# Performance work log

Hardware: AMD Instinct MI355X
Metric: run time of the kernel (lower is better)

The kernel has to match this reference:

```python
import jax, jax.numpy as jnp
import numpy as np

N = 100000
FEAT = 256
HID = 128
OUT = 64
E = 1600000


def setup_inputs() -> dict:
    key = jax.random.key(0)
    ks = jax.random.split(key, 8)
    x = jax.random.normal(ks[0], (N, FEAT), dtype=jnp.float32)
    edge_index = jax.random.randint(ks[1], (2, E), 0, N, dtype=jnp.int64)
    # Glorot-like weights, zero bias (PyG GCNConv default init style)
    def glorot(k, fin, fout):
        s = (6.0 / (fin + fout)) ** 0.5
        return jax.random.uniform(k, (fin, fout), jnp.float32, -s, s)
    return {
        "x": x,
        "edge_index": edge_index,
        "W1": glorot(ks[2], FEAT, HID), "b1": jnp.zeros((HID,), jnp.float32),
        "W2": glorot(ks[3], HID, HID), "b2": jnp.zeros((HID,), jnp.float32),
        "W3": glorot(ks[4], HID, OUT), "b3": jnp.zeros((OUT,), jnp.float32),
    }


def _gcn_prep(edge_index, n_nodes):
    # Add self-loops and compute symmetric normalization deg^-1/2 (PyG gcn_norm).
    loops = jnp.arange(n_nodes, dtype=edge_index.dtype)
    src = jnp.concatenate([edge_index[0], loops])
    dst = jnp.concatenate([edge_index[1], loops])
    ones = jnp.ones(src.shape[0], dtype=jnp.float32)
    deg = jax.ops.segment_sum(ones, dst, num_segments=n_nodes)
    dinv = jnp.where(deg > 0, jax.lax.rsqrt(jnp.maximum(deg, 1.0)), 0.0)
    norm = dinv[src] * dinv[dst]  # [E+N]
    return src, dst, norm


def _gcn_layer(x, src, dst, norm, W, b, n_nodes):
    h = x @ W                              # [N, F_out]
    msg = h[src] * norm[:, None]           # gather + edge scale
    out = jax.ops.segment_sum(msg, dst, num_segments=n_nodes)  # scatter-add
    return out + b


def reference(x, edge_index, W1, b1, W2, b2, W3, b3):
    n = x.shape[0]
    src, dst, norm = _gcn_prep(edge_index, n)
    h = jax.nn.relu(_gcn_layer(x, src, dst, norm, W1, b1, n))
    h = jax.nn.relu(_gcn_layer(h, src, dst, norm, W2, b2, n))
    return _gcn_layer(h, src, dst, norm, W3, b3, n)
```

## Files before the change

kernel.cpp:

```cpp
#include <hip/hip_runtime.h>
#include <hip/hip_bf16.h>


#define NNODES 100000
#define NB 391
#define PB 2048
#define BCAP 12288

typedef _Float16 half8  __attribute__((ext_vector_type(8)));
typedef _Float16 half4v __attribute__((ext_vector_type(4)));
typedef _Float16 half2v __attribute__((ext_vector_type(2)));
typedef float    floatx4 __attribute__((ext_vector_type(4)));

static __device__ __forceinline__ floatx4 h2f4(half4v v) {
    return (floatx4){(float)v.x, (float)v.y, (float)v.z, (float)v.w};
}

__global__ __launch_bounds__(256) void blockhist_k(const int* __restrict__ dst,
                                                   int* __restrict__ H, int e) {
    __shared__ int h[NB];
    for (int q = threadIdx.x; q < NB; q += 256) h[q] = 0;
    __syncthreads();
    int base = blockIdx.x * PB;
    int lim = e - base; if (lim > PB) lim = PB;
    for (int i = threadIdx.x; i < lim; i += 256)
        atomicAdd(&h[dst[base + i] >> 8], 1);
    __syncthreads();
    for (int q = threadIdx.x; q < NB; q += 256)
        H[(size_t)blockIdx.x * NB + q] = h[q];
}

__global__ __launch_bounds__(256) void bucketscan_k(const int* __restrict__ H,
                                                    int* __restrict__ O,
                                                    int* __restrict__ T, int npb) {
    __shared__ int lds[256];
    int b = blockIdx.x, t = threadIdx.x;
    int running = 0;
    for (int c0 = 0; c0 < npb; c0 += 256) {
        int idx = c0 + t;
        int v = (idx < npb) ? H[(size_t)idx * NB + b] : 0;
        lds[t] = v;
        __syncthreads();
        #pragma unroll
        for (int off = 1; off < 256; off <<= 1) {
            int u = (t >= off) ? lds[t - off] : 0;
            __syncthreads();
            lds[t] += u;
            __syncthreads();
        }
        int excl = lds[t] - v + running;
        if (idx < npb) O[(size_t)idx * NB + b] = excl;
        running += lds[255];
        __syncthreads();
    }
    if (t == 0) T[b] = running;
}

__global__ __launch_bounds__(512) void scanT_k(const int* __restrict__ T,
                                               int* __restrict__ bbase, int e) {
    __shared__ int lds[512];
    int t = threadIdx.x;
    int v = (t < NB) ? T[t] : 0;
    lds[t] = v;
    __syncthreads();
    #pragma unroll
    for (int off = 1; off < 512; off <<= 1) {
        int u = (t >= off) ? lds[t - off] : 0;
        __syncthreads();
        lds[t] += u;
        __syncthreads();
    }
    if (t < NB) bbase[t] = lds[t] - v;
    if (t == 0) bbase[NB] = e;
}

__global__ __launch_bounds__(256) void scatter_k(const int* __restrict__ src,
                                                 const int* __restrict__ dst,
                                                 const int* __restrict__ O,
                                                 const int* __restrict__ bbase,
                                                 unsigned* __restrict__ binned, int e) {
    __shared__ int cur[NB];
    for (int q = threadIdx.x; q < NB; q += 256)
        cur[q] = bbase[q] + O[(size_t)blockIdx.x * NB + q];
    __syncthreads();
    int base = blockIdx.x * PB;
    int lim = e - base; if (lim > PB) lim = PB;
    for (int i = threadIdx.x; i < lim; i += 256) {
        int d = dst[base + i];
        int s = src[base + i];
        int p = atomicAdd(&cur[d >> 8], 1);
        binned[p] = ((unsigned)(d & 255) << 17) | (unsigned)s;
    }
}

__global__ __launch_bounds__(256) void bucket_fill_k(
    const unsigned* __restrict__ binned, const int* __restrict__ bbase,
    int* __restrict__ rowptr, int* __restrict__ eidx,
    float* __restrict__ dinv, int n, int e) {
    __shared__ int cnt[256];
    __shared__ int cur[256];
    __shared__ int lds[256];
    __shared__ int sbuf[BCAP];
    int b = blockIdx.x, t = threadIdx.x;
    int beg = bbase[b], end = bbase[b + 1];
    int m = end - beg;
    cnt[t] = 0;
    __syncthreads();
    for (int q = t; q < m; q += 256) {
        unsigned r = binned[beg + q];
        atomicAdd(&cnt[r >> 17], 1);
    }
    __syncthreads();
    int v = cnt[t];
    lds[t] = v;
    __syncthreads();
    #pragma unroll
    for (int off = 1; off < 256; off <<= 1) {
        int u = (t >= off) ? lds[t - off] : 0;
        __syncthreads();
        lds[t] += u;
        __syncthreads();
    }
    int excl = lds[t] - v;
    int node = b * 256 + t;
    if (node < n) {
        rowptr[node] = beg + excl;
        dinv[node] = rsqrtf(1.0f + (float)v);
    }
    if (b == NB - 1 && t == 0) rowptr[n] = e;
    cur[t] = excl;
    __syncthreads();
    for (int q = t; q < m; q += 256) {
        unsigned r = binned[beg + q];
        int p = atomicAdd(&cur[r >> 17], 1);
        if (p < BCAP) sbuf[p] = (int)(r & 0x1FFFFu);
    }
    __syncthreads();
    for (int q = t; q < m; q += 256) eidx[beg + q] = sbuf[q];
}

__global__ __launch_bounds__(256) void castWt_k(
    const float* __restrict__ W1, const float* __restrict__ W2,
    const float* __restrict__ W3, _Float16* __restrict__ Wt1,
    _Float16* __restrict__ Wt2, _Float16* __restrict__ Wt3) {
    int i = blockIdx.x * 256 + threadIdx.x;
    if (i < 128 * 256) {
        int nn = i >> 8, k = i & 255;
        Wt1[i] = (_Float16)W1[k * 128 + nn];
    }
    if (i < 128 * 128) {
        int nn = i >> 7, k = i & 127;
        Wt2[i] = (_Float16)W2[k * 128 + nn];
    }
    if (i < 64 * 128) {
        int nn = i >> 7, k = i & 127;
        Wt3[i] = (_Float16)W3[k * 64 + nn];
    }
}

template<typename TA, int FIN, int FOUT>
__global__ __launch_bounds__(256) void gemm_mfma_k(
    const TA* __restrict__ X, const _Float16* __restrict__ Wt,
    const float* __restrict__ dinv, _Float16* __restrict__ G, int n)
{
    constexpr int KC = 64;
    constexpr int KP = 72;
    constexpr int NT = FOUT / 16;
    __shared__ _Float16 xS[128 * KP];

    const int tid  = threadIdx.x;
    const int wave = tid >> 6;
    const int lane = tid & 63;
    const int mrow = lane & 15;
    const int kq   = (lane >> 4) * 8;

    const int m0 = blockIdx.x * 128;
    const int row_s = tid >> 1;
    const int col_s = (tid & 1) * 32;
    int gr = m0 + row_s; if (gr > n - 1) gr = n - 1;

    floatx4 acc[2][NT];
    #pragma unroll
    for (int i = 0; i < 2; ++i)
        #pragma unroll
        for (int j = 0; j < NT; ++j) acc[i][j] = (floatx4){0.f, 0.f, 0.f, 0.f};

    const int lr0 = wave * 32 + mrow;
    const int lr1 = lr0 + 16;

    for (int kc = 0; kc < FIN; kc += KC) {
        if (kc) __syncthreads();
        _Float16* sp = &xS[row_s * KP + col_s];
        if constexpr (sizeof(TA) == 4) {
            const float* xp = (const float*)X + (size_t)gr * FIN + kc + col_s;
            #pragma unroll
            for (int q = 0; q < 4; ++q) {
                float4 u0 = *(const float4*)(xp + q * 8);
                float4 u1 = *(const float4*)(xp + q * 8 + 4);
                *(half8*)(sp + q * 8) =
                    (half8){(_Float16)u0.x, (_Float16)u0.y, (_Float16)u0.z, (_Float16)u0.w,
                            (_Float16)u1.x, (_Float16)u1.y, (_Float16)u1.z, (_Float16)u1.w};
            }
        } else {
            const _Float16* xp = (const _Float16*)X + (size_t)gr * FIN + kc + col_s;
            #pragma unroll
            for (int q = 0; q < 4; ++q)
                *(half8*)(sp + q * 8) = *(const half8*)(xp + q * 8);
        }
        __syncthreads();

        #pragma unroll
        for (int kk = 0; kk < KC; kk += 32) {
            half8 a0 = *(const half8*)&xS[lr0 * KP + kk + kq];
            half8 a1 = *(const half8*)&xS[lr1 * KP + kk + kq];
            #pragma unroll
            for (int ct = 0; ct < NT; ++ct) {
                half8 b = *(const half8*)(Wt + (size_t)(ct * 16 + mrow) * FIN + kc + kk + kq);
                acc[0][ct] = __builtin_amdgcn_mfma_f32_16x16x32_f16(a0, b, acc[0][ct], 0, 0, 0);
                acc[1][ct] = __builtin_amdgcn_mfma_f32_16x16x32_f16(a1, b, acc[1][ct], 0, 0, 0);
            }
        }
    }

    #pragma unroll
    for (int rt = 0; rt < 2; ++rt) {
        #pragma unroll
        for (int reg = 0; reg < 4; ++reg) {
            int r = m0 + wave * 32 + rt * 16 + (lane >> 4) * 4 + reg;
            if (r < n) {
                float s = dinv[r];
                #pragma unroll
                for (int ct = 0; ct < NT; ++ct) {
                    G[(size_t)r * FOUT + ct * 16 + mrow] = (_Float16)(acc[rt][ct][reg] * s);
                }
            }
        }
    }
}

template<bool RELU, typename OutT>
__global__ __launch_bounds__(256) void gather128_k(
    const _Float16* __restrict__ g, const int* __restrict__ rowptr,
    const int* __restrict__ eidx, const float* __restrict__ dinv,
    const float* __restrict__ bias, OutT* __restrict__ out, int n)
{
    int wave = threadIdx.x >> 6;
    int lane = threadIdx.x & 63;
    int half = lane >> 5;
    int hl   = lane & 31;
    int node = blockIdx.x * 4 + wave;
    if (node >= n) return;

    int beg = rowptr[node];
    int end = rowptr[node + 1];

    const half4v* g4 = (const half4v*)g;
    floatx4 aA = {0.f,0.f,0.f,0.f}, aB = aA, aC = aA, aD = aA;
    if (half == 0) aA = h2f4(g4[(size_t)node * 32 + hl]);

    for (int j0 = beg; j0 < end; j0 += 64) {
        int m = end - j0; if (m > 64) m = 64;
        int id = (lane < m) ? eidx[j0 + lane] : 0;
        int t = 0;
        for (; t + 7 < m; t += 8) {
            int i0 = __shfl(id, t + half);
            int i1 = __shfl(id, t + 2 + half);
            int i2 = __shfl(id, t + 4 + half);
            int i3 = __shfl(id, t + 6 + half);
            half4v v0 = g4[(size_t)i0 * 32 + hl];
            half4v v1 = g4[(size_t)i1 * 32 + hl];
            half4v v2 = g4[(size_t)i2 * 32 + hl];
            half4v v3 = g4[(size_t)i3 * 32 + hl];
            aA += h2f4(v0); aB += h2f4(v1); aC += h2f4(v2); aD += h2f4(v3);
        }
        for (; t + 1 < m; t += 2) {
            int i0 = __shfl(id, t + half);
            aA += h2f4(g4[(size_t)i0 * 32 + hl]);
        }
        if (t < m) {
            int i0 = __shfl(id, t);
            if (half == 0) aA += h2f4(g4[(size_t)i0 * 32 + hl]);
        }
    }
    aA += aB; aC += aD; aA += aC;
    aA.x += __shfl_down(aA.x, 32);
    aA.y += __shfl_down(aA.y, 32);
    aA.z += __shfl_down(aA.z, 32);
    aA.w += __shfl_down(aA.w, 32);

    if (half == 0) {
        float sc = dinv[node];
        float4 bb = *(const float4*)(bias + 4 * hl);
        float o0 = fmaf(aA.x, sc, bb.x);
        float o1 = fmaf(aA.y, sc, bb.y);
        float o2 = fmaf(aA.z, sc, bb.z);
        float o3 = fmaf(aA.w, sc, bb.w);
        if (RELU) {
            o0 = fmaxf(o0, 0.f); o1 = fmaxf(o1, 0.f);
            o2 = fmaxf(o2, 0.f); o3 = fmaxf(o3, 0.f);
        }
        if constexpr (sizeof(OutT) == 2) {
            ((half4v*)out)[(size_t)node * 32 + hl] =
                (half4v){(_Float16)o0, (_Float16)o1, (_Float16)o2, (_Float16)o3};
        } else {
            *(float4*)((float*)out + (size_t)node * 128 + 4 * hl) =
                make_float4(o0, o1, o2, o3);
        }
    }
}

template<bool RELU>
__global__ __launch_bounds__(256) void gather64_k(
    const _Float16* __restrict__ g, const int* __restrict__ rowptr,
    const int* __restrict__ eidx, const float* __restrict__ dinv,
    const float* __restrict__ bias, float* __restrict__ out, int n)
{
    int wave = threadIdx.x >> 6;
    int lane = threadIdx.x & 63;
    int half = lane >> 5;
    int hl   = lane & 31;
    int node = blockIdx.x * 4 + wave;
    if (node >= n) return;

    int beg = rowptr[node];
    int end = rowptr[node + 1];

    const half2v* g2 = (const half2v*)g;
    float ax=0.f, ay=0.f, bx=0.f, by=0.f, cx=0.f, cy=0.f, dx=0.f, dy=0.f;
    if (half == 0) {
        half2v v = g2[(size_t)node * 32 + hl];
        ax = (float)v.x; ay = (float)v.y;
    }

    for (int j0 = beg; j0 < end; j0 += 64) {
        int m = end - j0; if (m > 64) m = 64;
        int id = (lane < m) ? eidx[j0 + lane] : 0;
        int t = 0;
        for (; t + 7 < m; t += 8) {
            int i0 = __shfl(id, t + half);
            int i1 = __shfl(id, t + 2 + half);
            int i2 = __shfl(id, t + 4 + half);
            int i3 = __shfl(id, t + 6 + half);
            half2v v0 = g2[(size_t)i0 * 32 + hl];
            half2v v1 = g2[(size_t)i1 * 32 + hl];
            half2v v2 = g2[(size_t)i2 * 32 + hl];
            half2v v3 = g2[(size_t)i3 * 32 + hl];
            ax += (float)v0.x; ay += (float)v0.y;
            bx += (float)v1.x; by += (float)v1.y;
            cx += (float)v2.x; cy += (float)v2.y;
            dx += (float)v3.x; dy += (float)v3.y;
        }
        for (; t + 1 < m; t += 2) {
            int i0 = __shfl(id, t + half);
            half2v v0 = g2[(size_t)i0 * 32 + hl];
            ax += (float)v0.x; ay += (float)v0.y;
        }
        if (t < m) {
            int i0 = __shfl(id, t);
            if (half == 0) {
                half2v v0 = g2[(size_t)i0 * 32 + hl];
                ax += (float)v0.x; ay += (float)v0.y;
            }
        }
    }
    ax += bx + cx + dx; ay += by + cy + dy;
    ax += __shfl_down(ax, 32);
    ay += __shfl_down(ay, 32);

    if (half == 0) {
        float sc = dinv[node];
        float2 bb = *(const float2*)(bias + 2 * hl);
        float ox = fmaf(ax, sc, bb.x);
        float oy = fmaf(ay, sc, bb.y);
        if (RELU) { ox = fmaxf(ox, 0.f); oy = fmaxf(oy, 0.f); }
        *(float2*)(out + (size_t)node * 64 + 2 * hl) = make_float2(ox, oy);
    }
}

extern "C" void kernel_launch(void* const* d_in, const int* in_sizes, int n_in,
                              void* d_out, int out_size, void* d_ws, size_t ws_size,
                              hipStream_t stream) {
    const float* x  = (const float*)d_in[0];
    const int*   ei = (const int*)d_in[1];
    const float* W1 = (const float*)d_in[2];
    const float* b1 = (const float*)d_in[3];
    const float* W2 = (const float*)d_in[4];
    const float* b2 = (const float*)d_in[5];
    const float* W3 = (const float*)d_in[6];
    const float* b3 = (const float*)d_in[7];
    float* out = (float*)d_out;

    const int N = NNODES;
    const int E = in_sizes[1] / 2;
    const int* srcI = ei;
    const int* dstI = ei + E;

    const int npb = (E + PB - 1) / PB;

    char* ws = (char*)d_ws;
    size_t p = 0;
    auto alloc = [&](size_t bytes) { void* r = ws + p; p = (p + bytes + 255) & ~(size_t)255; return r; };
    float*     dinv   = (float*)    alloc((size_t)N * 4);
    int*       rowptr = (int*)      alloc((size_t)(N + 1) * 4);
    int*       bbase  = (int*)      alloc((size_t)(NB + 1) * 4);
    int*       T      = (int*)      alloc((size_t)NB * 4);
    int*       H      = (int*)      alloc((size_t)npb * NB * 4);
    int*       O      = (int*)      alloc((size_t)npb * NB * 4);
    unsigned*  binned = (unsigned*) alloc((size_t)E * 4);
    int*       eidx   = (int*)      alloc((size_t)E * 4);
    _Float16*  Wt1    = (_Float16*) alloc((size_t)128 * 256 * 2);
    _Float16*  Wt2    = (_Float16*) alloc((size_t)128 * 128 * 2);
    _Float16*  Wt3    = (_Float16*) alloc((size_t)64 * 128 * 2);
    _Float16*  A      = (_Float16*) alloc((size_t)N * 128 * 2);
    _Float16*  Ch     = (_Float16*) alloc((size_t)N * 128 * 2);

    const int nb_node4 = (N + 3) / 4;
    const int nb_gemm = (N + 127) / 128;

    blockhist_k<<<npb, 256, 0, stream>>>(dstI, H, E);
    castWt_k<<<128, 256, 0, stream>>>(W1, W2, W3, Wt1, Wt2, Wt3);
    bucketscan_k<<<NB, 256, 0, stream>>>(H, O, T, npb);
    scanT_k<<<1, 512, 0, stream>>>(T, bbase, E);
    scatter_k<<<npb, 256, 0, stream>>>(srcI, dstI, O, bbase, binned, E);
    bucket_fill_k<<<NB, 256, 0, stream>>>(binned, bbase, rowptr, eidx, dinv, N, E);

    gemm_mfma_k<float, 256, 128><<<nb_gemm, 256, 0, stream>>>(x, Wt1, dinv, A, N);
    gather128_k<true, _Float16><<<nb_node4, 256, 0, stream>>>(A, rowptr, eidx, dinv, b1, Ch, N);

    gemm_mfma_k<_Float16, 128, 128><<<nb_gemm, 256, 0, stream>>>(Ch, Wt2, dinv, A, N);
    gather128_k<true, _Float16><<<nb_node4, 256, 0, stream>>>(A, rowptr, eidx, dinv, b2, Ch, N);

    gemm_mfma_k<_Float16, 128, 64><<<nb_gemm, 256, 0, stream>>>(Ch, Wt3, dinv, A, N);
    gather64_k<false><<<nb_node4, 256, 0, stream>>>(A, rowptr, eidx, dinv, b3, out, N);
}
```

Before: 476.5 us.

## Replace LDS-staged GEMM with register-resident weight fragments and direct A loads

The dense transform kernel no longer stages X tiles through shared memory with barriers. Each wave now keeps its slice of the weight matrix in registers for the whole K range and splits the output columns across waves. Every wave loads its A fragments straight from global memory, with a one-step software prefetch. The block tile shrinks to 64 rows. This removes LDS traffic and __syncthreads, but all four waves now read the same A rows redundantly (relying on cache) and register pressure rises, especially for the FIN=256 layer with 16 half8 weight fragments per wave.

```diff
diff --git a/kernel.cpp b/kernel.cpp
--- a/kernel.cpp
+++ b/kernel.cpp
@@ -159,79 +159,84 @@
 }
 
 template<typename TA, int FIN, int FOUT>
-__global__ __launch_bounds__(256) void gemm_mfma_k(
+__global__ __launch_bounds__(256) void gemm_reg_k(
     const TA* __restrict__ X, const _Float16* __restrict__ Wt,
     const float* __restrict__ dinv, _Float16* __restrict__ G, int n)
 {
-    constexpr int KC = 64;
-    constexpr int KP = 72;
-    constexpr int NT = FOUT / 16;
-    __shared__ _Float16 xS[128 * KP];
-
+    constexpr int NCT = FOUT / 64;
+    constexpr int NKC = FIN / 32;
     const int tid  = threadIdx.x;
     const int wave = tid >> 6;
     const int lane = tid & 63;
     const int mrow = lane & 15;
     const int kq   = (lane >> 4) * 8;
-
-    const int m0 = blockIdx.x * 128;
-    const int row_s = tid >> 1;
-    const int col_s = (tid & 1) * 32;
-    int gr = m0 + row_s; if (gr > n - 1) gr = n - 1;
-
-    floatx4 acc[2][NT];
-    #pragma unroll
-    for (int i = 0; i < 2; ++i)
-        #pragma unroll
-        for (int j = 0; j < NT; ++j) acc[i][j] = (floatx4){0.f, 0.f, 0.f, 0.f};
-
-    const int lr0 = wave * 32 + mrow;
-    const int lr1 = lr0 + 16;
-
-    for (int kc = 0; kc < FIN; kc += KC) {
-        if (kc) __syncthreads();
-        _Float16* sp = &xS[row_s * KP + col_s];
-        if constexpr (sizeof(TA) == 4) {
-            const float* xp = (const float*)X + (size_t)gr * FIN + kc + col_s;
+    const int m0   = blockIdx.x * 64;
+
+    half8 bfr[NCT][NKC];
+    #pragma unroll
+    for (int ct = 0; ct < NCT; ++ct) {
+        const _Float16* wp = Wt + (size_t)((wave * NCT + ct) * 16 + mrow) * FIN + kq;
+        #pragma unroll
+        for (int kc = 0; kc < NKC; ++kc)
+            bfr[ct][kc] = *(const half8*)(wp + kc * 32);
+    }
+
+    const TA* ap[4];
+    #pragma unroll
+    for (int rt = 0; rt < 4; ++rt) {
+        int r = m0 + rt * 16 + mrow;
+        if (r > n - 1) r = n - 1;
+        ap[rt] = X + (size_t)r * FIN + kq;
+    }
+
+    auto lda = [&](const TA* p) -> half8 {
+        if constexpr (sizeof(TA) == 2) {
+            return *(const half8*)p;
+        } else {
+            float4 u0 = *(const float4*)p;
+            float4 u1 = *(const float4*)(p + 4);
+            return (half8){(_Float16)u0.x, (_Float16)u0.y, (_Float16)u0.z, (_Float16)u0.w,
+                           (_Float16)u1.x, (_Float16)u1.y, (_Float16)u1.z, (_Float16)u1.w};
+        }
+    };
+
+    floatx4 acc[4][NCT];
+    #pragma unroll
+    for (int rt = 0; rt < 4; ++rt)
+        #pragma unroll
+        for (int ct = 0; ct < NCT; ++ct) acc[rt][ct] = (floatx4){0.f, 0.f, 0.f, 0.f};
+
+    half8 a_cur[4], a_nxt[4];
+    #pragma unroll
+    for (int rt = 0; rt < 4; ++rt) a_cur[rt] = lda(ap[rt]);
+
+    #pragma unroll
+    for (int kc = 0; kc < NKC; ++kc) {
+        if (kc + 1 < NKC) {
             #pragma unroll
-            for (int q = 0; q < 4; ++q) {
-                float4 u0 = *(const float4*)(xp + q * 8);
-                float4 u1 = *(const float4*)(xp + q * 8 + 4);
-                *(half8*)(sp + q * 8) =
-                    (half8){(_Float16)u0.x, (_Float16)u0.y, (_Float16)u0.z, (_Float16)u0.w,
-                            (_Float16)u1.x, (_Float16)u1.y, (_Float16)u1.z, (_Float16)u1.w};
-            }
-        } else {
-            const _Float16* xp = (const _Float16*)X + (size_t)gr * FIN + kc + col_s;
+            for (int rt = 0; rt < 4; ++rt) a_nxt[rt] = lda(ap[rt] + (kc + 1) * 32);
+        }
+        #pragma unroll
+        for (int rt = 0; rt < 4; ++rt)
             #pragma unroll
-            for (int q = 0; q < 4; ++q)
-                *(half8*)(sp + q * 8) = *(const half8*)(xp + q * 8);
-        }
-        __syncthreads();
-
-        #pragma unroll
-        for (int kk = 0; kk < KC; kk += 32) {
-            half8 a0 = *(const half8*)&xS[lr0 * KP + kk + kq];
-            half8 a1 = *(const half8*)&xS[lr1 * KP + kk + kq];
-            #pragma unroll
-            for (int ct = 0; ct < NT; ++ct) {
-                half8 b = *(const half8*)(Wt + (size_t)(ct * 16 + mrow) * FIN + kc + kk + kq);
-                acc[0][ct] = __builtin_amdgcn_mfma_f32_16x16x32_f16(a0, b, acc[0][ct], 0, 0, 0);
-                acc[1][ct] = __builtin_amdgcn_mfma_f32_16x16x32_f16(a1, b, acc[1][ct], 0, 0, 0);
-            }
-        }
-    }
-
-    #pragma unroll
-    for (int rt = 0; rt < 2; ++rt) {
+            for (int ct = 0; ct < NCT; ++ct)
+                acc[rt][ct] = __builtin_amdgcn_mfma_f32_16x16x32_f16(
+                    a_cur[rt], bfr[ct][kc], acc[rt][ct], 0, 0, 0);
+        #pragma unroll
+        for (int rt = 0; rt < 4; ++rt) a_cur[rt] = a_nxt[rt];
+    }
+
+    #pragma unroll
+    for (int rt = 0; rt < 4; ++rt) {
         #pragma unroll
         for (int reg = 0; reg < 4; ++reg) {
-            int r = m0 + wave * 32 + rt * 16 + (lane >> 4) * 4 + reg;
+            int r = m0 + rt * 16 + (lane >> 4) * 4 + reg;
             if (r < n) {
                 float s = dinv[r];
                 #pragma unroll
-                for (int ct = 0; ct < NT; ++ct) {
-                    G[(size_t)r * FOUT + ct * 16 + mrow] = (_Float16)(acc[rt][ct][reg] * s);
+                for (int ct = 0; ct < NCT; ++ct) {
+                    G[(size_t)r * FOUT + (wave * NCT + ct) * 16 + mrow] =
+                        (_Float16)(acc[rt][ct][reg] * s);
                 }
             }
         }
@@ -415,7 +420,7 @@
     _Float16*  Ch     = (_Float16*) alloc((size_t)N * 128 * 2);
 
     const int nb_node4 = (N + 3) / 4;
-    const int nb_gemm = (N + 127) / 128;
+    const int nb_gemm = (N + 63) / 64;
 
     blockhist_k<<<npb, 256, 0, stream>>>(dstI, H, E);
     castWt_k<<<128, 256, 0, stream>>>(W1, W2, W3, Wt1, Wt2, Wt3);
@@ -424,12 +429,12 @@
     scatter_k<<<npb, 256, 0, stream>>>(srcI, dstI, O, bbase, binned, E);
     bucket_fill_k<<<NB, 256, 0, stream>>>(binned, bbase, rowptr, eidx, dinv, N, E);
 
-    gemm_mfma_k<float, 256, 128><<<nb_gemm, 256, 0, stream>>>(x, Wt1, dinv, A, N);
+    gemm_reg_k<float, 256, 128><<<nb_gemm, 256, 0, stream>>>(x, Wt1, dinv, A, N);
     gather128_k<true, _Float16><<<nb_node4, 256, 0, stream>>>(A, rowptr, eidx, dinv, b1, Ch, N);
 
-    gemm_mfma_k<_Float16, 128, 128><<<nb_gemm, 256, 0, stream>>>(Ch, Wt2, dinv, A, N);
+    gemm_reg_k<_Float16, 128, 128><<<nb_gemm, 256, 0, stream>>>(Ch, Wt2, dinv, A, N);
     gather128_k<true, _Float16><<<nb_node4, 256, 0, stream>>>(A, rowptr, eidx, dinv, b2, Ch, N);
 
-    gemm_mfma_k<_Float16, 128, 64><<<nb_gemm, 256, 0, stream>>>(Ch, Wt3, dinv, A, N);
+    gemm_reg_k<_Float16, 128, 64><<<nb_gemm, 256, 0, stream>>>(Ch, Wt3, dinv, A, N);
     gather64_k<false><<<nb_node4, 256, 0, stream>>>(A, rowptr, eidx, dinv, b3, out, N);
 }
```

Measured after the change: 488.5 us. 1.03x slower.
